# Performance work log

Hardware: AMD Instinct MI355X
Metric: run time of the kernel (lower is better)

Reference implementation:

```python
import jax, jax.numpy as jnp
import numpy as np

D_MODEL = 4096
NUM_EXPERTS = 64
TOP_K = 8


def setup_inputs() -> dict:
    key = jax.random.key(0)
    kx, kw = jax.random.split(key)
    x = jax.random.normal(kx, (4, 4096, D_MODEL), dtype=jnp.float32)
    # nn.Linear weight [num_experts, d_model]; y = x @ W.T
    W = jax.random.normal(kw, (NUM_EXPERTS, D_MODEL), dtype=jnp.float32) * (1.0 / np.sqrt(D_MODEL))
    return {"x": x, "W": W}


def reference(x, W):
    # logits: [b, s, e]
    logits = jnp.einsum('bsd,ed->bse', x, W)
    router_probs = jax.nn.softmax(logits, axis=-1)
    top_k_weights, top_k_indices = jax.lax.top_k(router_probs, TOP_K)
    top_k_weights = top_k_weights / (jnp.sum(top_k_weights, axis=-1, keepdims=True) + 1e-9)
    return top_k_weights, top_k_indices, router_probs
```

## Files before the change

### kernel.cpp

```cpp
#include <hip/hip_runtime.h>
#include <math.h>

#define D_MODEL 4096
#define NEXP    64
#define TOPK    8
#define NTOK    16384
#define BLK_TOK 64
#define DC      64
#define KSPLIT  4
#define KQ      (D_MODEL / KSPLIT)
#define NCHUNK_Q (KQ / DC)
#define EPW     8
#define NWAVE   (NEXP / EPW)
#define NTHR    (NWAVE * 64)

#define WT2_FLOATS (NEXP * D_MODEL)

typedef float v2f __attribute__((ext_vector_type(2)));

__global__ void transpose_w_kernel(const float* __restrict__ W, float* __restrict__ WT2) {
    int o = blockIdx.x * 256 + threadIdx.x;
    int p  = o & 1;
    int j  = (o >> 1) & 7;
    int d2 = (o >> 4) & 2047;
    int g  = o >> 15;
    WT2[o] = W[(size_t)(g * 8 + j) * D_MODEL + 2 * d2 + p];
}

__global__ __launch_bounds__(NTHR)
void router_kernel(const float* __restrict__ x, const float* __restrict__ WT2,
                   float* __restrict__ Pacc) {
    __shared__ __align__(16) float lds[2 * 4096];

    const int tid  = threadIdx.x;
    const int lane = tid & 63;
    const int g    = __builtin_amdgcn_readfirstlane(tid >> 6);
    const int s    = blockIdx.x & 3;
    const int tok0 = (blockIdx.x >> 2) * BLK_TOK;
    const int kbase = s * KQ;

    const int row  = tid >> 3;
    const int q    = tid & 7;

    v2f acc2[EPW];
#pragma unroll
    for (int j = 0; j < EPW; ++j) acc2[j] = (v2f)0.f;

    float4 xr[2];
    const float* xbase = x + (size_t)(tok0 + row) * D_MODEL + kbase + q * 4;
    const float* wk    = WT2 + (g << 15);

    auto load_chunk = [&](int d0) {
#pragma unroll
        for (int j = 0; j < 2; ++j)
            xr[j] = *(const float4*)(xbase + d0 + j * 32);
    };
    auto store_chunk = [&](int buf) {
#pragma unroll
        for (int j = 0; j < 2; ++j)
            *(float4*)&lds[buf * 4096 + (q + j * 8) * 256 + ((row ^ q) << 2)] = xr[j];
    };
    auto compute_chunk = [&](int buf, int kk) {
        const float* wc = wk + kbase * 8 + kk * (DC * 8);
        const float* xb = &lds[buf * 4096];
#pragma unroll 4
        for (int d4 = 0; d4 < DC / 4; ++d4) {
            const float4 xq = *(const float4*)(xb + d4 * 256 + (((lane ^ (d4 & 7))) << 2));
            const float* wd = wc + d4 * 32;
            const v2f xlo = {xq.x, xq.y};
            const v2f xhi = {xq.z, xq.w};
#pragma unroll
            for (int j = 0; j < EPW; ++j)
                acc2[j] = __builtin_elementwise_fma(xlo, *(const v2f*)(wd + j * 2), acc2[j]);
#pragma unroll
            for (int j = 0; j < EPW; ++j)
                acc2[j] = __builtin_elementwise_fma(xhi, *(const v2f*)(wd + 16 + j * 2), acc2[j]);
        }
    };

    load_chunk(0);
    store_chunk(0);
    __syncthreads();

    for (int kk = 0; kk < NCHUNK_Q; ++kk) {
        if (kk + 1 < NCHUNK_Q) load_chunk((kk + 1) * DC);
        compute_chunk(kk & 1, kk);
        if (kk + 1 < NCHUNK_Q) store_chunk((kk + 1) & 1);
        __syncthreads();
    }

    float* lg = lds;
#pragma unroll
    for (int j = 0; j < EPW; ++j)
        lg[lane * 65 + g * EPW + j] = acc2[j].x + acc2[j].y;
    __syncthreads();

    for (int i = tid; i < BLK_TOK * 16; i += NTHR) {
        const int t  = i >> 4;
        const int e4 = (i & 15) << 2;
        const float* src = &lg[t * 65 + e4];
        float* dst = &Pacc[(size_t)(tok0 + t) * NEXP + e4];
#pragma unroll
        for (int c = 0; c < 4; ++c) atomicAdd(dst + c, src[c]);
    }
}

__global__ __launch_bounds__(256)
void finalize_kernel(float* out_p, float* __restrict__ out_w, float* __restrict__ out_i,
                     int* __restrict__ cnt, int* __restrict__ list) {
    __shared__ float lg[BLK_TOK * 65];
    const int tid  = threadIdx.x;
    const int tok0 = blockIdx.x * BLK_TOK;

    for (int i = tid; i < BLK_TOK * 16; i += 256) {
        const int t  = i >> 4;
        const int e4 = (i & 15) << 2;
        const float4 a = *(const float4*)&out_p[(size_t)(tok0 + t) * NEXP + e4];
        float* dst = &lg[t * 65 + e4];
        dst[0] = a.x; dst[1] = a.y; dst[2] = a.z; dst[3] = a.w;
    }
    __syncthreads();

    if (tid < 64) {
        const int tok = tok0 + tid;
        float p[64];
        float m = -INFINITY;
#pragma unroll
        for (int e = 0; e < 64; ++e) {
            p[e] = lg[tid * 65 + e];
            m = fmaxf(m, p[e]);
        }
        float z = 0.f;
#pragma unroll
        for (int e = 0; e < 64; ++e) {
            p[e] = __expf(p[e] - m);
            z += p[e];
        }
        const float rz = 1.f / z;
#pragma unroll
        for (int e = 0; e < 64; ++e) {
            p[e] *= rz;
            lg[tid * 65 + e] = p[e];
        }

        float tv[9]; int ti[9];
#pragma unroll
        for (int k = 0; k < 9; ++k) { tv[k] = -1.f; ti[k] = 0; }
        for (int e = 0; e < 64; ++e) {
            float v = p[e]; int idx = e;
#pragma unroll
            for (int k = 0; k < 9; ++k) {
                const bool gt = v > tv[k];
                const float nv = gt ? v : tv[k];
                const int   ni = gt ? idx : ti[k];
                const float ov = gt ? tv[k] : v;
                const int   oi = gt ? ti[k] : idx;
                tv[k] = nv; ti[k] = ni; v = ov; idx = oi;
            }
        }
        int flag = 0;
#pragma unroll
        for (int k = 0; k < 8; ++k)
            if (tv[k] - tv[k + 1] <= tv[k] * 2e-4f + 1e-12f) flag = 1;
        if (flag) {
            int sidx = atomicAdd(cnt, 1);
            list[sidx] = tok;
        }

        float s8 = 0.f;
#pragma unroll
        for (int k = 0; k < 8; ++k) s8 += tv[k];
        const float denom = s8 + 1e-9f;
#pragma unroll
        for (int k = 0; k < 8; ++k) {
            out_w[tok * TOPK + k] = tv[k] / denom;
            out_i[tok * TOPK + k] = (float)ti[k];
        }
    }
    __syncthreads();

    for (int i = tid; i < BLK_TOK * 16; i += 256) {
        const int t  = i >> 4;
        const int e4 = (i & 15) << 2;
        const float* src = &lg[t * 65 + e4];
        *(float4*)&out_p[(size_t)(tok0 + t) * NEXP + e4] =
            make_float4(src[0], src[1], src[2], src[3]);
    }
}

__global__ __launch_bounds__(256)
void repair_kernel(const float* __restrict__ x, const float* __restrict__ W,
                   const int* __restrict__ cnt, const int* __restrict__ list,
                   float* __restrict__ out_w, float* __restrict__ out_i) {
    __shared__ float  xs[D_MODEL];
    __shared__ double ls[4][NEXP];
    const int tid = threadIdx.x;
    const int e   = tid & 63;
    const int w4  = tid >> 6;
    const int n   = cnt[0];

    for (int i = blockIdx.x; i < n; i += gridDim.x) {
        const int tok = list[i];
        __syncthreads();
        const float4* xsrc = (const float4*)(x + (size_t)tok * D_MODEL);
        for (int v = tid; v < D_MODEL / 4; v += 256)
            ((float4*)xs)[v] = xsrc[v];
        __syncthreads();

        const float* wrow = W + (size_t)e * D_MODEL + w4 * (D_MODEL / 4);
        const float* xrow = xs + w4 * (D_MODEL / 4);
        double s0 = 0., s1 = 0., s2 = 0., s3 = 0.;
        for (int d = 0; d < D_MODEL / 4; d += 4) {
            const float4 wv = *(const float4*)(wrow + d);
            const float4 xv = *(const float4*)(xrow + d);
            s0 += (double)xv.x * (double)wv.x;
            s1 += (double)xv.y * (double)wv.y;
            s2 += (double)xv.z * (double)wv.z;
            s3 += (double)xv.w * (double)wv.w;
        }
        ls[w4][e] = (s0 + s1) + (s2 + s3);
        __syncthreads();

        if (tid == 0) {
            double lsum[64];
            for (int k = 0; k < 64; ++k)
                lsum[k] = (ls[0][k] + ls[1][k]) + (ls[2][k] + ls[3][k]);
            double m = -1e300;
            for (int k = 0; k < 64; ++k) m = lsum[k] > m ? lsum[k] : m;
            double p[64], Z = 0.;
            for (int k = 0; k < 64; ++k) { p[k] = exp(lsum[k] - m); Z += p[k]; }
            for (int k = 0; k < 64; ++k) p[k] /= Z;

            double tv[8]; int ti[8];
            for (int k = 0; k < 8; ++k) { tv[k] = -1.; ti[k] = 0; }
            for (int k = 0; k < 64; ++k) {
                double v = p[k]; int idx = k;
                for (int u = 0; u < 8; ++u) {
                    const bool gt = v > tv[u];
                    const double nv = gt ? v : tv[u];
                    const int    ni = gt ? idx : ti[u];
                    const double ov = gt ? tv[u] : v;
                    const int    oi = gt ? ti[u] : idx;
                    tv[u] = nv; ti[u] = ni; v = ov; idx = oi;
                }
            }
            double s8 = 0.;
            for (int k = 0; k < 8; ++k) s8 += tv[k];
            const double denom = s8 + 1e-9;
            for (int k = 0; k < 8; ++k) {
                out_w[tok * TOPK + k] = (float)(tv[k] / denom);
                out_i[tok * TOPK + k] = (float)ti[k];
            }
        }
    }
}

extern "C" void kernel_launch(void* const* d_in, const int* in_sizes, int n_in,
                              void* d_out, int out_size, void* d_ws, size_t ws_size,
                              hipStream_t stream) {
    const float* x = (const float*)d_in[0];
    const float* W = (const float*)d_in[1];

    float* WT2  = (float*)d_ws;
    int*   cnt  = (int*)((float*)d_ws + WT2_FLOATS);
    int*   list = cnt + 1;

    float* out   = (float*)d_out;
    float* out_w = out;
    float* out_i = out + NTOK * TOPK;
    float* out_p = out + 2 * NTOK * TOPK;

    hipMemsetAsync(cnt, 0, sizeof(int), stream);
    hipMemsetAsync(out_p, 0, (size_t)NTOK * NEXP * sizeof(float), stream);
    transpose_w_kernel<<<WT2_FLOATS / 256, 256, 0, stream>>>(W, WT2);
    router_kernel<<<(NTOK / BLK_TOK) * KSPLIT, NTHR, 0, stream>>>(x, WT2, out_p);
    finalize_kernel<<<NTOK / BLK_TOK, 256, 0, stream>>>(out_p, out_w, out_i, cnt, list);
    repair_kernel<<<256, 256, 0, stream>>>(x, W, cnt, list, out_w, out_i);
}
```

Baseline: 560.3 us.

## Fold output zeroing into transpose kernel and use scalar FMA weight layout

Removes the two hipMemsetAsync calls and zeroes the probability accumulator and counter inside the weight transpose kernel, saving launch overhead. The transposed weight layout changes from interleaved pairs to eight contiguous experts per d, and the router inner loop switches from packed two-wide FMAs to scalar fmaf with a broadcast x. This simplifies the indexing but may lose packed FP32 FMA throughput.

Result: no change. 555.4 us (-0.9%).

```diff
diff --git a/kernel.cpp b/kernel.cpp
--- a/kernel.cpp
+++ b/kernel.cpp
@@ -16,15 +16,15 @@
 
 #define WT2_FLOATS (NEXP * D_MODEL)
 
-typedef float v2f __attribute__((ext_vector_type(2)));
-
-__global__ void transpose_w_kernel(const float* __restrict__ W, float* __restrict__ WT2) {
+__global__ void transpose_w_kernel(const float* __restrict__ W, float* __restrict__ WT2,
+                                   float* __restrict__ out_p, int* __restrict__ cnt) {
     int o = blockIdx.x * 256 + threadIdx.x;
-    int p  = o & 1;
-    int j  = (o >> 1) & 7;
-    int d2 = (o >> 4) & 2047;
-    int g  = o >> 15;
-    WT2[o] = W[(size_t)(g * 8 + j) * D_MODEL + 2 * d2 + p];
+    int j = o & 7;
+    int d = (o >> 3) & (D_MODEL - 1);
+    int g = o >> 15;
+    WT2[o] = W[(size_t)(g * 8 + j) * D_MODEL + d];
+    *(float4*)&out_p[(size_t)o * 4] = make_float4(0.f, 0.f, 0.f, 0.f);
+    if (o == 0) *cnt = 0;
 }
 
 __global__ __launch_bounds__(NTHR)
@@ -42,9 +42,9 @@
     const int row  = tid >> 3;
     const int q    = tid & 7;
 
-    v2f acc2[EPW];
-#pragma unroll
-    for (int j = 0; j < EPW; ++j) acc2[j] = (v2f)0.f;
+    float acc[EPW];
+#pragma unroll
+    for (int j = 0; j < EPW; ++j) acc[j] = 0.f;
 
     float4 xr[2];
     const float* xbase = x + (size_t)(tok0 + row) * D_MODEL + kbase + q * 4;
@@ -61,20 +61,19 @@
             *(float4*)&lds[buf * 4096 + (q + j * 8) * 256 + ((row ^ q) << 2)] = xr[j];
     };
     auto compute_chunk = [&](int buf, int kk) {
-        const float* wc = wk + kbase * 8 + kk * (DC * 8);
+        const float* wc = wk + (kbase + kk * DC) * 8;
         const float* xb = &lds[buf * 4096];
 #pragma unroll 4
         for (int d4 = 0; d4 < DC / 4; ++d4) {
-            const float4 xq = *(const float4*)(xb + d4 * 256 + (((lane ^ (d4 & 7))) << 2));
+            const float4 xq = *(const float4*)(xb + d4 * 256 + ((lane ^ (d4 & 7)) << 2));
             const float* wd = wc + d4 * 32;
-            const v2f xlo = {xq.x, xq.y};
-            const v2f xhi = {xq.z, xq.w};
-#pragma unroll
-            for (int j = 0; j < EPW; ++j)
-                acc2[j] = __builtin_elementwise_fma(xlo, *(const v2f*)(wd + j * 2), acc2[j]);
-#pragma unroll
-            for (int j = 0; j < EPW; ++j)
-                acc2[j] = __builtin_elementwise_fma(xhi, *(const v2f*)(wd + 16 + j * 2), acc2[j]);
+#pragma unroll
+            for (int dd = 0; dd < 4; ++dd) {
+                const float xv = (dd == 0) ? xq.x : (dd == 1) ? xq.y : (dd == 2) ? xq.z : xq.w;
+#pragma unroll
+                for (int j = 0; j < 8; ++j)
+                    acc[j] = fmaf(xv, wd[dd * 8 + j], acc[j]);
+            }
         }
     };
 
@@ -92,7 +91,7 @@
     float* lg = lds;
 #pragma unroll
     for (int j = 0; j < EPW; ++j)
-        lg[lane * 65 + g * EPW + j] = acc2[j].x + acc2[j].y;
+        lg[lane * 65 + g * EPW + j] = acc[j];
     __syncthreads();
 
     for (int i = tid; i < BLK_TOK * 16; i += NTHR) {
@@ -270,9 +269,7 @@
     float* out_i = out + NTOK * TOPK;
     float* out_p = out + 2 * NTOK * TOPK;
 
-    hipMemsetAsync(cnt, 0, sizeof(int), stream);
-    hipMemsetAsync(out_p, 0, (size_t)NTOK * NEXP * sizeof(float), stream);
-    transpose_w_kernel<<<WT2_FLOATS / 256, 256, 0, stream>>>(W, WT2);
+    transpose_w_kernel<<<WT2_FLOATS / 256, 256, 0, stream>>>(W, WT2, out_p, cnt);
     router_kernel<<<(NTOK / BLK_TOK) * KSPLIT, NTHR, 0, stream>>>(x, WT2, out_p);
     finalize_kernel<<<NTOK / BLK_TOK, 256, 0, stream>>>(out_p, out_w, out_i, cnt, list);
     repair_kernel<<<256, 256, 0, stream>>>(x, W, cnt, list, out_w, out_i);
```
